# Kernel optimization log

Hardware: AMD Instinct MI355X
Metric: run time of the kernel (lower is better)

## Reference

```python
import jax, jax.numpy as jnp
import numpy as np

HEADS = 16
EMBED = 1024
HEAD_DIM = EMBED // HEADS


def setup_inputs() -> dict:
    key = jax.random.key(0)
    ks = jax.random.split(key, 10)
    B, SQ, SKV = 2, 2048, 2048
    s = 1.0 / np.sqrt(HEAD_DIM)
    sd = 1.0 / np.sqrt(EMBED)
    return {
        "queries": jax.random.normal(ks[0], (B, SQ, EMBED), jnp.float32),
        "values": jax.random.normal(ks[1], (B, SKV, EMBED), jnp.float32),
        "heads": HEADS,
        "Wv": jax.random.normal(ks[2], (HEAD_DIM, HEAD_DIM), jnp.float32) * s,
        "bv": jax.random.normal(ks[3], (HEAD_DIM,), jnp.float32) * 0.02,
        "Wk": jax.random.normal(ks[4], (HEAD_DIM, HEAD_DIM), jnp.float32) * s,
        "bk": jax.random.normal(ks[5], (HEAD_DIM,), jnp.float32) * 0.02,
        "Wq": jax.random.normal(ks[6], (HEAD_DIM, HEAD_DIM), jnp.float32) * s,
        "bq": jax.random.normal(ks[7], (HEAD_DIM,), jnp.float32) * 0.02,
        "Wd": jax.random.normal(ks[8], (EMBED, EMBED), jnp.float32) * sd,
        "bd": jax.random.normal(ks[9], (EMBED,), jnp.float32) * 0.02,
    }


def reference(queries, values, heads, Wv, bv, Wk, bk, Wq, bq, Wd, bd):
    n, sq, e = queries.shape
    skv = values.shape[1]
    d = e // heads
    # reshape to per-head layout [b, s, h, d]
    q_in = queries.reshape(n, sq, heads, d)
    v_in = values.reshape(n, skv, heads, d)
    # shared per-head linear projections (torch Linear: x @ W.T + b)
    v = jnp.einsum("bshd,ed->bshe", v_in, Wv) + bv
    # quirk preserved: keys computed from the ALREADY-PROJECTED values
    k = jnp.einsum("bshd,ed->bshe", v, Wk) + bk
    q = jnp.einsum("bshd,ed->bshe", q_in, Wq) + bq
    # full O(n^2) score matrix [b, h, sq, skv] (as in source)
    scores = jnp.einsum("bqhd,bkhd->bhqk", q, k) / jnp.sqrt(jnp.asarray(d, q.dtype))
    attn = jax.nn.softmax(scores, axis=-1)
    out = jnp.einsum("bhqk,bkhd->bqhd", attn, v).reshape(n, sq, e)
    return out @ Wd.T + bd
```

## Files before the change

### kernel.cpp

```cpp
#include <hip/hip_runtime.h>
#include <hip/hip_bf16.h>
#include <hip/hip_fp16.h>
#include <math.h>

typedef _Float16 f16;
typedef _Float16 f16x8 __attribute__((ext_vector_type(8)));
typedef _Float16 f16x4 __attribute__((ext_vector_type(4)));
typedef _Float16 f16x2 __attribute__((ext_vector_type(2)));
typedef unsigned short u16x8v __attribute__((ext_vector_type(8)));
typedef float f32x4 __attribute__((ext_vector_type(4)));

namespace {
constexpr int B = 2;
constexpr int H = 16;
constexpr int S = 2048;
constexpr int D = 64;
constexpr int E = 1024;
constexpr int LP = 72;
constexpr float QSCALE = 0.125f * 1.4426950408889634f;
}

__global__ void make_wkv(const float* __restrict__ Wk, const float* __restrict__ Wv,
                         const float* __restrict__ bv, const float* __restrict__ bk,
                         float* __restrict__ Wkv, float* __restrict__ bkv) {
  const int g = blockIdx.x * 256 + threadIdx.x;
  const int i = g >> 6, j = g & 63;
  float s = 0.f;
#pragma unroll 16
  for (int d = 0; d < 64; ++d) s = fmaf(Wk[i * 64 + d], Wv[d * 64 + j], s);
  Wkv[g] = s;
  if (g < 64) {
    float bb = bk[g];
#pragma unroll 16
    for (int d = 0; d < 64; ++d) bb = fmaf(Wk[g * 64 + d], bv[d], bb);
    bkv[g] = bb;
  }
}

__global__ __launch_bounds__(256) void cvt_wd(const float* __restrict__ W, f16* __restrict__ out) {
  const int i = blockIdx.x * 256 + threadIdx.x;
  const float4 f = ((const float4*)W)[i];
  f16x4 o;
  o.x = (f16)f.x; o.y = (f16)f.y; o.z = (f16)f.z; o.w = (f16)f.w;
  *(f16x4*)(out + 4 * (size_t)i) = o;
}

__global__ __launch_bounds__(256) void proj_mfma(const float* __restrict__ x,
                                                 const float* __restrict__ W,
                                                 const float* __restrict__ bias,
                                                 f16* __restrict__ out, float scale) {
  const int t = threadIdx.x, lane = t & 63, w = t >> 6;
  const int l15 = lane & 15, quad = lane >> 4;
  const int m0 = (blockIdx.x * 4 + w) * 64;

  f16x8 wf[4][2], af[4][2];
#pragma unroll
  for (int nt = 0; nt < 4; ++nt)
#pragma unroll
    for (int kc = 0; kc < 2; ++kc) {
      const float* g = W + (size_t)(nt * 16 + l15) * 64 + kc * 32 + quad * 8;
      const float4 a = *(const float4*)g, b2 = *(const float4*)(g + 4);
      f16x8 v;
      v[0]=(f16)a.x; v[1]=(f16)a.y; v[2]=(f16)a.z; v[3]=(f16)a.w;
      v[4]=(f16)b2.x; v[5]=(f16)b2.y; v[6]=(f16)b2.z; v[7]=(f16)b2.w;
      wf[nt][kc] = v;
    }
#pragma unroll
  for (int mt = 0; mt < 4; ++mt)
#pragma unroll
    for (int kc = 0; kc < 2; ++kc) {
      const float* g = x + (size_t)(m0 + mt * 16 + l15) * 64 + kc * 32 + quad * 8;
      const float4 a = *(const float4*)g, b2 = *(const float4*)(g + 4);
      f16x8 v;
      v[0]=(f16)a.x; v[1]=(f16)a.y; v[2]=(f16)a.z; v[3]=(f16)a.w;
      v[4]=(f16)b2.x; v[5]=(f16)b2.y; v[6]=(f16)b2.z; v[7]=(f16)b2.w;
      af[mt][kc] = v;
    }

  f32x4 acc[4][4];
#pragma unroll
  for (int mt = 0; mt < 4; ++mt)
#pragma unroll
    for (int nt = 0; nt < 4; ++nt) acc[mt][nt] = (f32x4){0.f, 0.f, 0.f, 0.f};
#pragma unroll
  for (int kc = 0; kc < 2; ++kc)
#pragma unroll
    for (int nt = 0; nt < 4; ++nt)
#pragma unroll
      for (int mt = 0; mt < 4; ++mt)
        acc[mt][nt] = __builtin_amdgcn_mfma_f32_16x16x32_f16(af[mt][kc], wf[nt][kc], acc[mt][nt], 0, 0, 0);

  float bl[4];
#pragma unroll
  for (int nt = 0; nt < 4; ++nt) bl[nt] = bias[nt * 16 + l15];

#pragma unroll
  for (int mt = 0; mt < 4; ++mt)
#pragma unroll
    for (int r = 0; r < 4; ++r) {
      const int g = m0 + mt * 16 + quad * 4 + r;
      const int h = g & 15, bs = g >> 4;
      const int b = bs >> 11, s = bs & 2047;
      f16* o = out + ((size_t)(b * H + h) * S + s) * 64;
#pragma unroll
      for (int nt = 0; nt < 4; ++nt)
        o[nt * 16 + l15] = (f16)((acc[mt][nt][r] + bl[nt]) * scale);
    }
}

__global__ __launch_bounds__(256) void attn_mfma(const f16* __restrict__ qp,
                                                 const f16* __restrict__ kp,
                                                 const f16* __restrict__ vp,
                                                 f16* __restrict__ ao) {
  __shared__ f16 ks[64 * LP];
  __shared__ f16 vt[64 * LP];
  __shared__ f16 ps[4 * 32 * LP];
  const int t = threadIdx.x, lane = t & 63, w = t >> 6;
  const int l15 = lane & 15, quad = lane >> 4;
  const int bh = blockIdx.x;
  const int q0 = blockIdx.y * 128;
  const f16* qbase = qp + ((size_t)bh * S + q0 + w * 32) * D;
  const f16* kbase = kp + (size_t)bh * S * D;
  const f16* vbase = vp + (size_t)bh * S * D;
  f16* pw = ps + w * 32 * LP;

  f16x8 qf[2][2];
#pragma unroll
  for (int mt = 0; mt < 2; ++mt)
#pragma unroll
    for (int kc = 0; kc < 2; ++kc)
      qf[mt][kc] = *(const f16x8*)(qbase + (size_t)(mt * 16 + l15) * D + kc * 32 + quad * 8);

  f16x8 vb4;
#pragma unroll
  for (int j = 0; j < 8; ++j) vb4[j] = (l15 == 0) ? (f16)1.0f : (f16)0.0f;

  f32x4 O[2][5];
#pragma unroll
  for (int mt = 0; mt < 2; ++mt)
#pragma unroll
    for (int nt = 0; nt < 5; ++nt) O[mt][nt] = (f32x4){0.f, 0.f, 0.f, 0.f};

  for (int kt = 0; kt < S / 64; ++kt) {
    __syncthreads();
    {
      const int r = t >> 2, c0 = (t & 3) * 16;
      const f16* g = kbase + ((size_t)kt * 64 + r) * D + c0;
      *(f16x8*)&ks[r * LP + c0] = *(const f16x8*)g;
      *(f16x8*)&ks[r * LP + c0 + 8] = *(const f16x8*)(g + 8);
    }
    {
      const int d0 = (t >> 5) * 8, pc0 = (t & 31) * 2;
      const int kva = (pc0 & 3) * 16 + (pc0 >> 2);
      const u16x8v a = *(const u16x8v*)(vbase + ((size_t)kt * 64 + kva) * D + d0);
      const u16x8v b2 = *(const u16x8v*)(vbase + ((size_t)kt * 64 + kva + 16) * D + d0);
#pragma unroll
      for (int j = 0; j < 8; ++j) {
        const unsigned pk = (unsigned)a[j] | ((unsigned)b2[j] << 16);
        *(unsigned*)&vt[(d0 + j) * LP + pc0] = pk;
      }
    }
    __syncthreads();

    f32x4 sc[2][4];
#pragma unroll
    for (int mt = 0; mt < 2; ++mt)
#pragma unroll
      for (int nt = 0; nt < 4; ++nt) sc[mt][nt] = (f32x4){0.f, 0.f, 0.f, 0.f};
#pragma unroll
    for (int kc = 0; kc < 2; ++kc)
#pragma unroll
      for (int nt = 0; nt < 4; ++nt) {
        const f16x8 bf = *(const f16x8*)&ks[(nt * 16 + l15) * LP + kc * 32 + quad * 8];
#pragma unroll
        for (int mt = 0; mt < 2; ++mt)
          sc[mt][nt] = __builtin_amdgcn_mfma_f32_16x16x32_f16(qf[mt][kc], bf, sc[mt][nt], 0, 0, 0);
      }

#pragma unroll
    for (int mt = 0; mt < 2; ++mt)
#pragma unroll
      for (int r = 0; r < 4; ++r) {
        const float p0 = __builtin_amdgcn_exp2f(sc[mt][0][r]);
        const float p1 = __builtin_amdgcn_exp2f(sc[mt][1][r]);
        const float p2 = __builtin_amdgcn_exp2f(sc[mt][2][r]);
        const float p3 = __builtin_amdgcn_exp2f(sc[mt][3][r]);
        union { f16x4 v4; f16x2 h[2]; } u;
        u.h[0] = __builtin_bit_cast(f16x2, __builtin_amdgcn_cvt_pkrtz(p0, p1));
        u.h[1] = __builtin_bit_cast(f16x2, __builtin_amdgcn_cvt_pkrtz(p2, p3));
        *(f16x4*)&pw[(mt * 16 + quad * 4 + r) * LP + l15 * 4] = u.v4;
      }
    __asm__ volatile("s_waitcnt lgkmcnt(0)" ::: "memory");

    f16x8 pa[2][2];
#pragma unroll
    for (int mt = 0; mt < 2; ++mt)
#pragma unroll
      for (int kc = 0; kc < 2; ++kc)
        pa[mt][kc] = *(const f16x8*)&pw[(mt * 16 + l15) * LP + kc * 32 + quad * 8];
#pragma unroll
    for (int kc = 0; kc < 2; ++kc) {
#pragma unroll
      for (int nt = 0; nt < 4; ++nt) {
        const f16x8 vbf = *(const f16x8*)&vt[(nt * 16 + l15) * LP + kc * 32 + quad * 8];
#pragma unroll
        for (int mt = 0; mt < 2; ++mt)
          O[mt][nt] = __builtin_amdgcn_mfma_f32_16x16x32_f16(pa[mt][kc], vbf, O[mt][nt], 0, 0, 0);
      }
#pragma unroll
      for (int mt = 0; mt < 2; ++mt)
        O[mt][4] = __builtin_amdgcn_mfma_f32_16x16x32_f16(pa[mt][kc], vb4, O[mt][4], 0, 0, 0);
    }
  }

  const int b = bh >> 4, h = bh & 15;
#pragma unroll
  for (int mt = 0; mt < 2; ++mt)
#pragma unroll
    for (int r = 0; r < 4; ++r) {
      const float l = __shfl(O[mt][4][r], quad << 4, 64);
      const float inv = 1.f / l;
      const int row = q0 + w * 32 + mt * 16 + quad * 4 + r;
      f16* o = ao + ((size_t)b * S + row) * E + h * D;
#pragma unroll
      for (int nt = 0; nt < 4; ++nt)
        o[nt * 16 + l15] = (f16)(O[mt][nt][r] * inv);
    }
}

__global__ __launch_bounds__(256) void dense_mfma(const f16* __restrict__ A,
                                                  const f16* __restrict__ Wd16,
                                                  const float* __restrict__ bd,
                                                  float* __restrict__ out) {
  __shared__ f16 as[128 * LP];
  __shared__ f16 bs[128 * LP];
  const int t = threadIdx.x;
  const int lane = t & 63;
  const int w = t >> 6;
  const int l15 = lane & 15;
  const int quad = lane >> 4;
  const int m0 = blockIdx.x * 128;
  const int n0 = blockIdx.y * 128;
  const int wm = (w >> 1) * 64, wn = (w & 1) * 64;

  f32x4 acc[4][4];
#pragma unroll
  for (int mt = 0; mt < 4; ++mt)
#pragma unroll
    for (int nt = 0; nt < 4; ++nt) acc[mt][nt] = (f32x4){0.f, 0.f, 0.f, 0.f};

  for (int kt = 0; kt < E / 64; ++kt) {
    __syncthreads();
    {
      const int r = t >> 1, c0 = (t & 1) * 32;
      const f16* ga = A + (size_t)(m0 + r) * E + kt * 64 + c0;
      const f16* gb = Wd16 + (size_t)(n0 + r) * E + kt * 64 + c0;
#pragma unroll
      for (int c = 0; c < 4; ++c) {
        *(f16x8*)&as[r * LP + c0 + 8 * c] = *(const f16x8*)(ga + 8 * c);
        *(f16x8*)&bs[r * LP + c0 + 8 * c] = *(const f16x8*)(gb + 8 * c);
      }
    }
    __syncthreads();
    f16x8 af[4][2];
#pragma unroll
    for (int mt = 0; mt < 4; ++mt)
#pragma unroll
      for (int kc = 0; kc < 2; ++kc)
        af[mt][kc] = *(const f16x8*)&as[(wm + mt * 16 + l15) * LP + kc * 32 + quad * 8];
#pragma unroll
    for (int kc = 0; kc < 2; ++kc)
#pragma unroll
      for (int nt = 0; nt < 4; ++nt) {
        const f16x8 bf = *(const f16x8*)&bs[(wn + nt * 16 + l15) * LP + kc * 32 + quad * 8];
#pragma unroll
        for (int mt = 0; mt < 4; ++mt)
          acc[mt][nt] = __builtin_amdgcn_mfma_f32_16x16x32_f16(af[mt][kc], bf, acc[mt][nt], 0, 0, 0);
      }
  }
#pragma unroll
  for (int nt = 0; nt < 4; ++nt) {
    const int col = n0 + wn + nt * 16 + l15;
    const float bdv = bd[col];
#pragma unroll
    for (int mt = 0; mt < 4; ++mt)
#pragma unroll
      for (int r = 0; r < 4; ++r)
        out[(size_t)(m0 + wm + mt * 16 + quad * 4 + r) * E + col] = acc[mt][nt][r] + bdv;
  }
}

extern "C" void kernel_launch(void* const* d_in, const int* in_sizes, int n_in,
                              void* d_out, int out_size, void* d_ws, size_t ws_size,
                              hipStream_t stream) {
  const float* queries = (const float*)d_in[0];
  const float* values  = (const float*)d_in[1];
  const float* Wv = (const float*)d_in[3];
  const float* bv = (const float*)d_in[4];
  const float* Wk = (const float*)d_in[5];
  const float* bk = (const float*)d_in[6];
  const float* Wq = (const float*)d_in[7];
  const float* bq = (const float*)d_in[8];
  const float* Wd = (const float*)d_in[9];
  const float* bd = (const float*)d_in[10];
  float* out = (float*)d_out;

  char* ws = (char*)d_ws;
  f16* qp    = (f16*)(ws);
  f16* kp    = (f16*)(ws + 8u * 1024 * 1024);
  f16* vp    = (f16*)(ws + 16u * 1024 * 1024);
  f16* ao    = (f16*)(ws + 24u * 1024 * 1024);
  f16* wd16  = (f16*)(ws + 32u * 1024 * 1024);
  float* wkv = (float*)(ws + 34u * 1024 * 1024);
  float* bkv = (float*)(ws + 34u * 1024 * 1024 + 16384);
  (void)ws_size; (void)in_sizes; (void)n_in; (void)out_size;

  make_wkv<<<16, 256, 0, stream>>>(Wk, Wv, bv, bk, wkv, bkv);
  cvt_wd<<<E * E / 1024, 256, 0, stream>>>(Wd, wd16);
  proj_mfma<<<256, 256, 0, stream>>>(queries, Wq, bq, qp, QSCALE);
  proj_mfma<<<256, 256, 0, stream>>>(values, Wv, bv, vp, 1.0f);
  proj_mfma<<<256, 256, 0, stream>>>(values, wkv, bkv, kp, 1.0f);
  attn_mfma<<<dim3(B * H, S / 128), 256, 0, stream>>>(qp, kp, vp, ao);
  dense_mfma<<<dim3(B * S / 128, E / 128), 256, 0, stream>>>(ao, wd16, bd, out);
}
```

Measured before the change: 197.9 us.

## Double-buffer K/V tiles in attention and merge three projection launches

The attention kernel now prefetches the next K/V tile into registers during the current tile's compute and writes it into a second LDS buffer. This cuts the loop from two barriers to one, so global load latency can overlap the MFMA work. s_setprio raises wave priority around the MFMA blocks. The three projection launches become one launch with a blockIdx.y selector, which removes launch overhead. The cost is more LDS and registers, which may lower occupancy.

New measurement: 187.3 us. -5.4%, faster.

```diff
diff --git a/kernel.cpp b/kernel.cpp
--- a/kernel.cpp
+++ b/kernel.cpp
@@ -45,10 +45,24 @@
   *(f16x4*)(out + 4 * (size_t)i) = o;
 }
 
-__global__ __launch_bounds__(256) void proj_mfma(const float* __restrict__ x,
-                                                 const float* __restrict__ W,
-                                                 const float* __restrict__ bias,
-                                                 f16* __restrict__ out, float scale) {
+__global__ __launch_bounds__(256) void proj3_mfma(const float* __restrict__ xq,
+                                                  const float* __restrict__ xv,
+                                                  const float* __restrict__ Wq,
+                                                  const float* __restrict__ bq,
+                                                  const float* __restrict__ Wv,
+                                                  const float* __restrict__ bv,
+                                                  const float* __restrict__ Wkv,
+                                                  const float* __restrict__ bkv,
+                                                  f16* __restrict__ qp,
+                                                  f16* __restrict__ vp,
+                                                  f16* __restrict__ kp) {
+  const int which = blockIdx.y;
+  const float* x    = (which == 0) ? xq : xv;
+  const float* W    = (which == 0) ? Wq : (which == 1) ? Wv : Wkv;
+  const float* bias = (which == 0) ? bq : (which == 1) ? bv : bkv;
+  f16* out          = (which == 0) ? qp : (which == 1) ? vp : kp;
+  const float scale = (which == 0) ? QSCALE : 1.0f;
+
   const int t = threadIdx.x, lane = t & 63, w = t >> 6;
   const int l15 = lane & 15, quad = lane >> 4;
   const int m0 = (blockIdx.x * 4 + w) * 64;
@@ -112,8 +126,8 @@
                                                  const f16* __restrict__ kp,
                                                  const f16* __restrict__ vp,
                                                  f16* __restrict__ ao) {
-  __shared__ f16 ks[64 * LP];
-  __shared__ f16 vt[64 * LP];
+  __shared__ f16 ks[2][64 * LP];
+  __shared__ f16 vt[2][64 * LP];
   __shared__ f16 ps[4 * 32 * LP];
   const int t = threadIdx.x, lane = t & 63, w = t >> 6;
   const int l15 = lane & 15, quad = lane >> 4;
@@ -124,6 +138,10 @@
   const f16* vbase = vp + (size_t)bh * S * D;
   f16* pw = ps + w * 32 * LP;
 
+  const int kr = t >> 2, kc0 = (t & 3) * 16;
+  const int vd0 = (t >> 5) * 8, vpc0 = (t & 31) * 2;
+  const int vkva = (vpc0 & 3) * 16 + (vpc0 >> 2);
+
   f16x8 qf[2][2];
 #pragma unroll
   for (int mt = 0; mt < 2; ++mt)
@@ -141,41 +159,55 @@
 #pragma unroll
     for (int nt = 0; nt < 5; ++nt) O[mt][nt] = (f32x4){0.f, 0.f, 0.f, 0.f};
 
+  u16x8v ka, kb2, va, vb2;
+  {
+    const f16* gk = kbase + (size_t)kr * D + kc0;
+    ka  = *(const u16x8v*)gk;
+    kb2 = *(const u16x8v*)(gk + 8);
+    const f16* gv = vbase + (size_t)vkva * D + vd0;
+    va  = *(const u16x8v*)gv;
+    vb2 = *(const u16x8v*)(gv + 16 * D);
+  }
+  {
+    *(u16x8v*)&ks[0][kr * LP + kc0]     = ka;
+    *(u16x8v*)&ks[0][kr * LP + kc0 + 8] = kb2;
+#pragma unroll
+    for (int j = 0; j < 8; ++j) {
+      const unsigned pk = (unsigned)va[j] | ((unsigned)vb2[j] << 16);
+      *(unsigned*)&vt[0][(vd0 + j) * LP + vpc0] = pk;
+    }
+  }
+
+  int cur = 0;
   for (int kt = 0; kt < S / 64; ++kt) {
-    __syncthreads();
-    {
-      const int r = t >> 2, c0 = (t & 3) * 16;
-      const f16* g = kbase + ((size_t)kt * 64 + r) * D + c0;
-      *(f16x8*)&ks[r * LP + c0] = *(const f16x8*)g;
-      *(f16x8*)&ks[r * LP + c0 + 8] = *(const f16x8*)(g + 8);
-    }
-    {
-      const int d0 = (t >> 5) * 8, pc0 = (t & 31) * 2;
-      const int kva = (pc0 & 3) * 16 + (pc0 >> 2);
-      const u16x8v a = *(const u16x8v*)(vbase + ((size_t)kt * 64 + kva) * D + d0);
-      const u16x8v b2 = *(const u16x8v*)(vbase + ((size_t)kt * 64 + kva + 16) * D + d0);
-#pragma unroll
-      for (int j = 0; j < 8; ++j) {
-        const unsigned pk = (unsigned)a[j] | ((unsigned)b2[j] << 16);
-        *(unsigned*)&vt[(d0 + j) * LP + pc0] = pk;
-      }
-    }
-    __syncthreads();
+    if (kt + 1 < S / 64) {
+      const f16* gk = kbase + ((size_t)(kt + 1) * 64 + kr) * D + kc0;
+      ka  = *(const u16x8v*)gk;
+      kb2 = *(const u16x8v*)(gk + 8);
+      const f16* gv = vbase + ((size_t)(kt + 1) * 64 + vkva) * D + vd0;
+      va  = *(const u16x8v*)gv;
+      vb2 = *(const u16x8v*)(gv + 16 * D);
+    }
+    __asm__ volatile("s_waitcnt lgkmcnt(0)" ::: "memory");
+    __builtin_amdgcn_s_barrier();
+    __asm__ volatile("" ::: "memory");
 
     f32x4 sc[2][4];
 #pragma unroll
     for (int mt = 0; mt < 2; ++mt)
 #pragma unroll
       for (int nt = 0; nt < 4; ++nt) sc[mt][nt] = (f32x4){0.f, 0.f, 0.f, 0.f};
+    __builtin_amdgcn_s_setprio(1);
 #pragma unroll
     for (int kc = 0; kc < 2; ++kc)
 #pragma unroll
       for (int nt = 0; nt < 4; ++nt) {
-        const f16x8 bf = *(const f16x8*)&ks[(nt * 16 + l15) * LP + kc * 32 + quad * 8];
+        const f16x8 bf = *(const f16x8*)&ks[cur][(nt * 16 + l15) * LP + kc * 32 + quad * 8];
 #pragma unroll
         for (int mt = 0; mt < 2; ++mt)
           sc[mt][nt] = __builtin_amdgcn_mfma_f32_16x16x32_f16(qf[mt][kc], bf, sc[mt][nt], 0, 0, 0);
       }
+    __builtin_amdgcn_s_setprio(0);
 
 #pragma unroll
     for (int mt = 0; mt < 2; ++mt)
@@ -198,11 +230,12 @@
 #pragma unroll
       for (int kc = 0; kc < 2; ++kc)
         pa[mt][kc] = *(const f16x8*)&pw[(mt * 16 + l15) * LP + kc * 32 + quad * 8];
+    __builtin_amdgcn_s_setprio(1);
 #pragma unroll
     for (int kc = 0; kc < 2; ++kc) {
 #pragma unroll
       for (int nt = 0; nt < 4; ++nt) {
-        const f16x8 vbf = *(const f16x8*)&vt[(nt * 16 + l15) * LP + kc * 32 + quad * 8];
+        const f16x8 vbf = *(const f16x8*)&vt[cur][(nt * 16 + l15) * LP + kc * 32 + quad * 8];
 #pragma unroll
         for (int mt = 0; mt < 2; ++mt)
           O[mt][nt] = __builtin_amdgcn_mfma_f32_16x16x32_f16(pa[mt][kc], vbf, O[mt][nt], 0, 0, 0);
@@ -211,6 +244,19 @@
       for (int mt = 0; mt < 2; ++mt)
         O[mt][4] = __builtin_amdgcn_mfma_f32_16x16x32_f16(pa[mt][kc], vb4, O[mt][4], 0, 0, 0);
     }
+    __builtin_amdgcn_s_setprio(0);
+
+    if (kt + 1 < S / 64) {
+      const int nb = cur ^ 1;
+      *(u16x8v*)&ks[nb][kr * LP + kc0]     = ka;
+      *(u16x8v*)&ks[nb][kr * LP + kc0 + 8] = kb2;
+#pragma unroll
+      for (int j = 0; j < 8; ++j) {
+        const unsigned pk = (unsigned)va[j] | ((unsigned)vb2[j] << 16);
+        *(unsigned*)&vt[nb][(vd0 + j) * LP + vpc0] = pk;
+      }
+    }
+    cur ^= 1;
   }
 
   const int b = bh >> 4, h = bh & 15;
@@ -317,9 +363,7 @@
 
   make_wkv<<<16, 256, 0, stream>>>(Wk, Wv, bv, bk, wkv, bkv);
   cvt_wd<<<E * E / 1024, 256, 0, stream>>>(Wd, wd16);
-  proj_mfma<<<256, 256, 0, stream>>>(queries, Wq, bq, qp, QSCALE);
-  proj_mfma<<<256, 256, 0, stream>>>(values, Wv, bv, vp, 1.0f);
-  proj_mfma<<<256, 256, 0, stream>>>(values, wkv, bkv, kp, 1.0f);
+  proj3_mfma<<<dim3(256, 3), 256, 0, stream>>>(queries, values, Wq, bq, Wv, bv, wkv, bkv, qp, vp, kp);
   attn_mfma<<<dim3(B * H, S / 128), 256, 0, stream>>>(qp, kp, vp, ao);
   dense_mfma<<<dim3(B * S / 128, E / 128), 256, 0, stream>>>(ao, wd16, bd, out);
 }
```
